# Performance work log

Measured on AMD Instinct MI355X. Metric: run time of the kernel, lower is better.

Reference implementation:

```python
import jax, jax.numpy as jnp
import numpy as np

B, T, D = 2, 2048, 2048
NH, NKV, HD = 16, 4, 128
EPS = 1e-6
ROPE_THETA = 10000.0


def rms_norm(x, w):
    # per-head RMSNorm over the last (head_dim) axis
    var = jnp.mean(jnp.square(x), axis=-1, keepdims=True)
    return x * jax.lax.rsqrt(var + EPS) * w


def rope_sin_cos(seq_len, dim, dtype):
    inv_freq = 1.0 / (ROPE_THETA ** (jnp.arange(0, dim, 2, dtype=jnp.float32) / dim))
    t = jnp.arange(seq_len, dtype=jnp.float32)
    ang = jnp.outer(t, inv_freq)                      # [T, HD/2]
    ang = jnp.concatenate([ang, ang], axis=-1)         # [T, HD]
    return jnp.sin(ang).astype(dtype), jnp.cos(ang).astype(dtype)


def rotate_half(x):
    x1, x2 = jnp.split(x, 2, axis=-1)
    return jnp.concatenate([-x2, x1], axis=-1)


def apply_rope(x, sin, cos):
    # x: [B, T, H, HD]; sin/cos: [T, HD]
    s = sin[None, :, None, :]
    c = cos[None, :, None, :]
    return x * c + rotate_half(x) * s


def setup_inputs() -> dict:
    key = jax.random.key(0)
    ks = jax.random.split(key, 5)
    scale = 1.0 / np.sqrt(D)
    return {
        "x": jax.random.normal(ks[0], (B, T, D), jnp.float32),
        "wq": jax.random.normal(ks[1], (D, D), jnp.float32) * scale,
        "wk": jax.random.normal(ks[2], (NKV * HD, D), jnp.float32) * scale,
        "wv": jax.random.normal(ks[3], (NKV * HD, D), jnp.float32) * scale,
        "wo": jax.random.normal(ks[4], (D, D), jnp.float32) * scale,
        "q_norm_w": jnp.ones((HD,), jnp.float32),
        "k_norm_w": jnp.ones((HD,), jnp.float32),
    }


def reference(x, wq, wk, wv, wo, q_norm_w, k_norm_w):
    b, t, _ = x.shape
    q = (x @ wq.T).reshape(b, t, NH, HD)    # [B,T,NH,HD]
    k = (x @ wk.T).reshape(b, t, NKV, HD)   # [B,T,NKV,HD]
    v = (x @ wv.T).reshape(b, t, NKV, HD)

    # per-head QK RMS norm
    q = rms_norm(q, q_norm_w)
    k = rms_norm(k, k_norm_w)

    # RoPE
    sin, cos = rope_sin_cos(t, HD, x.dtype)
    q = apply_rope(q, sin, cos)
    k = apply_rope(k, sin, cos)

    # GQA: expand kv heads to match query heads
    rep = NH // NKV
    k = jnp.repeat(k, rep, axis=2)          # [B,T,NH,HD]
    v = jnp.repeat(v, rep, axis=2)

    # causal SDPA
    scale = 1.0 / np.sqrt(HD)
    scores = jnp.einsum('bqhd,bkhd->bhqk', q, k) * scale
    causal = jnp.tril(jnp.ones((t, t), bool))
    scores = jnp.where(causal[None, None], scores, jnp.finfo(scores.dtype).min)
    probs = jax.nn.softmax(scores, axis=-1)
    att = jnp.einsum('bhqk,bkhd->bqhd', probs, v).reshape(b, t, NH * HD)
    return att @ wo.T
```

## Files before the change

### kernel.cpp

```cpp
#include <hip/hip_runtime.h>
#include <hip/hip_bf16.h>

#define B_ 2
#define T_ 2048
#define D_ 2048
#define NH_ 16
#define NKV_ 4
#define HD_ 128

using bf16 = __bf16;
using bf16x8 = __attribute__((ext_vector_type(8))) __bf16;
using bf16x4 = __attribute__((ext_vector_type(4))) __bf16;
using f32x4 = __attribute__((ext_vector_type(4))) float;

__device__ __forceinline__ void gld_lds16(bf16* lds, const bf16* g) {
  __builtin_amdgcn_global_load_lds(
      (const __attribute__((address_space(1))) void*)g,
      (__attribute__((address_space(3))) void*)lds, 16, 0, 0);
}

__global__ __launch_bounds__(256) void cvt_all(const float* __restrict__ x,
                                               const float* __restrict__ wq,
                                               const float* __restrict__ wk,
                                               const float* __restrict__ wv,
                                               const float* __restrict__ wo,
                                               bf16* __restrict__ xb,
                                               bf16* __restrict__ wqkvb,
                                               bf16* __restrict__ wob) {
  const int bid = blockIdx.x;
  const float* src;
  bf16* dst;
  int base;
  if (bid < 8192)       { src = x;  dst = xb;              base = bid; }
  else if (bid < 12288) { src = wq; dst = wqkvb;           base = bid - 8192; }
  else if (bid < 13312) { src = wk; dst = wqkvb + 4194304; base = bid - 12288; }
  else if (bid < 14336) { src = wv; dst = wqkvb + 5242880; base = bid - 13312; }
  else                  { src = wo; dst = wob;             base = bid - 14336; }
  const int i = base * 256 + threadIdx.x;
  float4 v = ((const float4*)src)[i];
  bf16x4 o;
  o[0] = (bf16)v.x; o[1] = (bf16)v.y; o[2] = (bf16)v.z; o[3] = (bf16)v.w;
  ((bf16x4*)dst)[i] = o;
}

template<typename OutT>
__global__ __launch_bounds__(256) void gemm_bt(const bf16* __restrict__ A,
                                               const bf16* __restrict__ Bt,
                                               OutT* __restrict__ C,
                                               int M, int N, int K) {
  __shared__ bf16 As[3][128 * 32];
  __shared__ bf16 Bs[3][128 * 32];
  const int tid = threadIdx.x;
  const int wid = tid >> 6;
  const int lane = tid & 63;
  const int g = lane >> 4, r = lane & 15;
  const int wm = wid >> 1, wn = wid & 1;
  const int gx = gridDim.x;
  const int nwg = gx * gridDim.y;
  const int flat = blockIdx.y * gx + blockIdx.x;
  const int swz = (flat & 7) * (nwg >> 3) + (flat >> 3);
  const long bm = (long)(swz / gx) * 128, bn = (long)(swz % gx) * 128;
  f32x4 acc[4][4] = {};
  const int NT = K >> 5;

  auto stage = [&](int buf, int k0) {
    for (int c = 0; c < 2; ++c) {
      int ch = wid * 2 + c;
      int row = ch * 16 + (lane >> 2);
      int col = (lane & 3) * 8;
      gld_lds16(&As[buf][ch * 512], A + (bm + row) * K + k0 + col);
      gld_lds16(&Bs[buf][ch * 512], Bt + (bn + row) * K + k0 + col);
    }
  };

  stage(0, 0);
  stage(1, 32);
  for (int t = 0; t < NT; ++t) {
    if (t + 1 < NT)
      asm volatile("s_waitcnt vmcnt(4)" ::: "memory");
    else
      asm volatile("s_waitcnt vmcnt(0)" ::: "memory");
    __builtin_amdgcn_s_barrier();
    if (t + 2 < NT) stage((t + 2) % 3, (t + 2) * 32);
    const bf16* as = As[t % 3];
    const bf16* bs = Bs[t % 3];
    bf16x8 af[4], bfr[4];
    for (int m = 0; m < 4; ++m)
      af[m] = *(const bf16x8*)(as + (wm * 64 + m * 16 + r) * 32 + g * 8);
    for (int n = 0; n < 4; ++n)
      bfr[n] = *(const bf16x8*)(bs + (wn * 64 + n * 16 + r) * 32 + g * 8);
    for (int m = 0; m < 4; ++m)
      for (int n = 0; n < 4; ++n)
        acc[m][n] = __builtin_amdgcn_mfma_f32_16x16x32_bf16(af[m], bfr[n], acc[m][n], 0, 0, 0);
  }

  for (int m = 0; m < 4; ++m)
    for (int n = 0; n < 4; ++n)
      for (int e = 0; e < 4; ++e) {
        long row = bm + wm * 64 + m * 16 + g * 4 + e;
        long col = bn + wn * 64 + n * 16 + r;
        C[row * N + col] = (OutT)acc[m][n][e];
      }
}

template<int IS_K>
__global__ __launch_bounds__(256) void norm_rope(const bf16* __restrict__ qkv,
                                                 const float* __restrict__ w,
                                                 bf16* __restrict__ out) {
  const int lane = threadIdx.x & 63;
  const int rloc = threadIdx.x >> 6;
  const int NHH = IS_K ? NKV_ : NH_;
  const int COFF = IS_K ? 2048 : 0;
  const long rid = (long)blockIdx.x * 4 + rloc;
  const int h = (int)(rid % NHH);
  const long bt = rid / NHH;
  const int t = (int)(bt % T_);
  const bf16* src = qkv + bt * 3072 + COFF + h * HD_;
  float v0 = (float)src[lane];
  float v1 = (float)src[lane + 64];
  float ss = v0 * v0 + v1 * v1;
  for (int o = 1; o < 64; o <<= 1) ss += __shfl_xor(ss, o, 64);
  float inv = rsqrtf(ss * (1.f / HD_) + 1e-6f);
  float n0 = v0 * inv * w[lane];
  float n1 = v1 * inv * w[lane + 64];
  float ang = (float)t * exp2f((float)lane * (-13.287712379549449f / 64.f));
  float sv, cv;
  __sincosf(ang, &sv, &cv);
  float o0 = n0 * cv - n1 * sv;
  float o1 = n1 * cv + n0 * sv;
  bf16* dst;
  if (IS_K) {
    long b = bt / T_;
    dst = out + ((b * NKV_ + h) * (long)T_ + t) * HD_;
  } else {
    dst = out + (bt * NH_ + h) * HD_;
  }
  dst[lane] = (bf16)o0;
  dst[lane + 64] = (bf16)o1;
}

__global__ __launch_bounds__(256) void vpack(const bf16* __restrict__ qkv,
                                             bf16* __restrict__ Vt) {
  __shared__ float tile[64][65];
  const int tt = blockIdx.x;
  const int dd = blockIdx.y & 1;
  const int bkv = blockIdx.y >> 1;
  const long b = bkv >> 2;
  const int kv = bkv & 3;
  const int t0 = tt * 64, d0 = dd * 64;
  for (int i = 0; i < 2; ++i) {
    int row = i * 32 + (threadIdx.x >> 3);
    int c8 = (threadIdx.x & 7) * 8;
    bf16x8 v = *(const bf16x8*)&qkv[(b * T_ + t0 + row) * 3072 + 2560 + kv * HD_ + d0 + c8];
    for (int j = 0; j < 8; ++j) tile[row][c8 + j] = (float)v[j];
  }
  __syncthreads();
  for (int i = 0; i < 2; ++i) {
    int drow = i * 32 + (threadIdx.x >> 3);
    int tc8 = (threadIdx.x & 7) * 8;
    bf16x8 o;
    for (int j = 0; j < 8; ++j) o[j] = (bf16)tile[tc8 + j][drow];
    *(bf16x8*)&Vt[((b * NKV_ + kv) * (long)HD_ + d0 + drow) * T_ + t0 + tc8] = o;
  }
}

__global__ __launch_bounds__(512) void flash_attn(const bf16* __restrict__ Q,
                                                  const bf16* __restrict__ K,
                                                  const bf16* __restrict__ V,
                                                  bf16* __restrict__ O) {
  __shared__ bf16 Ks[2][64 * 128];
  __shared__ bf16 Vs[2][128 * 64];
  __shared__ bf16 Ps[8][16 * 64];
  const int h = blockIdx.y, b = blockIdx.z;
  const int qt = b ? blockIdx.x : (gridDim.x - 1) - blockIdx.x;
  const int kv = h >> 2;
  const int tid = threadIdx.x, wid = tid >> 6, lane = tid & 63;
  const int g = lane >> 4, r = lane & 15;
  const int q0 = qt * 128;
  const int qbase = q0 + wid * 16;
  const int q = qbase + r;

  bf16x8 aq[4];
  const bf16* qp = Q + ((long)(b * T_ + q)) * (NH_ * HD_) + h * HD_;
  for (int kk = 0; kk < 4; ++kk) aq[kk] = *(const bf16x8*)(qp + kk * 32 + g * 8);

  f32x4 oacc[8] = {};
  float m_run = -1e30f, l_run = 0.f;

  const bf16* Kbase = K + ((long)(b * NKV_ + kv)) * T_ * HD_;
  const bf16* Vbase = V + ((long)(b * NKV_ + kv)) * (long)HD_ * T_;
  const int nkt = 2 * qt + 2;

  auto stageKV = [&](int buf, int k0) {
    for (int c = 0; c < 2; ++c) {
      int ch = wid * 2 + c;
      {
        int row = ch * 4 + (lane >> 4);
        int srccol = ((lane & 15) ^ (row & 7)) * 8;
        gld_lds16(&Ks[buf][ch * 512], Kbase + (long)(k0 + row) * HD_ + srccol);
      }
      {
        int row = ch * 8 + (lane >> 3);
        int srccol = ((lane & 7) ^ (row & 7)) * 8;
        gld_lds16(&Vs[buf][ch * 512], Vbase + (long)row * T_ + k0 + srccol);
      }
    }
  };

  stageKV(0, 0);
  for (int kt = 0; kt < nkt; ++kt) {
    const int k0 = kt * 64;
    const int cur = kt & 1;
    if (kt + 1 < nkt) {
      stageKV(cur ^ 1, k0 + 64);
      asm volatile("s_waitcnt vmcnt(4)" ::: "memory");
    } else {
      asm volatile("s_waitcnt vmcnt(0)" ::: "memory");
    }
    __builtin_amdgcn_s_barrier();

    f32x4 s[4] = {};
    __builtin_amdgcn_s_setprio(1);
    for (int n = 0; n < 4; ++n)
      for (int kk = 0; kk < 4; ++kk) {
        int row = n * 16 + r;
        bf16x8 bk = *(const bf16x8*)(&Ks[cur][row * 128 + (((kk * 4 + g) ^ (row & 7)) * 8)]);
        s[n] = __builtin_amdgcn_mfma_f32_16x16x32_bf16(bk, aq[kk], s[n], 0, 0, 0);
      }
    __builtin_amdgcn_s_setprio(0);

    const float scale = 0.088388347648318447f;
    const bool domask = (k0 + 63 > qbase);
    float mx = -1e30f;
    if (domask) {
      for (int n = 0; n < 4; ++n) {
        const int km = k0 + n * 16 + g * 4;
        for (int e = 0; e < 4; ++e) {
          float v = s[n][e] * scale;
          if (km + e > q) v = -1e30f;
          s[n][e] = v;
          mx = fmaxf(mx, v);
        }
      }
    } else {
      for (int n = 0; n < 4; ++n)
        for (int e = 0; e < 4; ++e) {
          float v = s[n][e] * scale;
          s[n][e] = v;
          mx = fmaxf(mx, v);
        }
    }
    mx = fmaxf(mx, __shfl_xor(mx, 16, 64));
    mx = fmaxf(mx, __shfl_xor(mx, 32, 64));
    float mnew = fmaxf(m_run, mx);
    float alpha = __expf(m_run - mnew);
    float ls = 0.f;
    for (int n = 0; n < 4; ++n) {
      bf16x4 pb;
      for (int e = 0; e < 4; ++e) {
        float p = __expf(s[n][e] - mnew);
        ls += p;
        pb[e] = (bf16)p;
      }
      int c = n * 2 + (g >> 1);
      *(bf16x4*)(&Ps[wid][r * 64 + ((c ^ (r & 7)) * 8) + (g & 1) * 4]) = pb;
    }
    ls += __shfl_xor(ls, 16, 64);
    ls += __shfl_xor(ls, 32, 64);
    m_run = mnew;
    l_run = l_run * alpha + ls;

    float al[4];
    for (int e = 0; e < 4; ++e)
      al[e] = __shfl(alpha, (lane & 48) | (g * 4 + e), 64);
    for (int dt = 0; dt < 8; ++dt)
      for (int e = 0; e < 4; ++e) oacc[dt][e] *= al[e];

    asm volatile("s_waitcnt lgkmcnt(0)" ::: "memory");

    __builtin_amdgcn_s_setprio(1);
    for (int kk = 0; kk < 2; ++kk) {
      bf16x8 ap = *(const bf16x8*)(&Ps[wid][r * 64 + (((kk * 4 + g) ^ (r & 7)) * 8)]);
      for (int dt = 0; dt < 8; ++dt) {
        int row = dt * 16 + r;
        bf16x8 bv = *(const bf16x8*)(&Vs[cur][row * 64 + (((kk * 4 + g) ^ (row & 7)) * 8)]);
        oacc[dt] = __builtin_amdgcn_mfma_f32_16x16x32_bf16(ap, bv, oacc[dt], 0, 0, 0);
      }
    }
    __builtin_amdgcn_s_setprio(0);
    __builtin_amdgcn_s_barrier();
  }

  float li[4];
  for (int e = 0; e < 4; ++e) {
    float lv = __shfl(l_run, (lane & 48) | (g * 4 + e), 64);
    li[e] = 1.f / lv;
  }
  for (int e = 0; e < 4; ++e) {
    const int grow = q0 + wid * 16 + g * 4 + e;
    bf16* dst = O + ((long)(b * T_ + grow)) * (NH_ * HD_) + h * HD_;
    for (int dt = 0; dt < 8; ++dt)
      dst[dt * 16 + r] = (bf16)(oacc[dt][e] * li[e]);
  }
}

extern "C" void kernel_launch(void* const* d_in, const int* in_sizes, int n_in,
                              void* d_out, int out_size, void* d_ws, size_t ws_size,
                              hipStream_t stream) {
  const float* x  = (const float*)d_in[0];
  const float* wq = (const float*)d_in[1];
  const float* wk = (const float*)d_in[2];
  const float* wv = (const float*)d_in[3];
  const float* wo = (const float*)d_in[4];
  const float* qw = (const float*)d_in[5];
  const float* kw = (const float*)d_in[6];
  float* out = (float*)d_out;

  char* p = (char*)d_ws;
  bf16* xb    = (bf16*)(p);
  bf16* wqkvb = (bf16*)(p + 16777216);
  bf16* wob   = (bf16*)(p + 29360128);
  bf16* QKVr  = (bf16*)(p + 37748736);
  bf16* Qb    = (bf16*)(p + 62914560);
  bf16* Kb    = (bf16*)(p + 79691776);
  bf16* Vt    = (bf16*)(p + 83886080);
  bf16* attb  = (bf16*)(p + 88080384);

  cvt_all<<<18432, 256, 0, stream>>>(x, wq, wk, wv, wo, xb, wqkvb, wob);

  gemm_bt<bf16><<<dim3(24, 32), 256, 0, stream>>>(xb, wqkvb, QKVr, 4096, 3072, 2048);

  norm_rope<0><<<16384, 256, 0, stream>>>(QKVr, qw, Qb);
  norm_rope<1><<<4096, 256, 0, stream>>>(QKVr, kw, Kb);
  vpack<<<dim3(32, 16), 256, 0, stream>>>(QKVr, Vt);

  flash_attn<<<dim3(16, 16, 2), 512, 0, stream>>>(Qb, Kb, Vt, attb);

  gemm_bt<float><<<dim3(16, 32), 256, 0, stream>>>(attb, wob, out, 4096, 2048, 2048);
}
```

Before: 218.0 us.

## Split flash-attn softmax into two half-tile passes and merge Q/K norm-rope launches

Result: slower. 224.9 us (+3.2%).

```diff
diff --git a/kernel.cpp b/kernel.cpp
--- a/kernel.cpp
+++ b/kernel.cpp
@@ -103,15 +103,19 @@
       }
 }
 
-template<int IS_K>
-__global__ __launch_bounds__(256) void norm_rope(const bf16* __restrict__ qkv,
-                                                 const float* __restrict__ w,
-                                                 bf16* __restrict__ out) {
+__global__ __launch_bounds__(256) void norm_rope_qk(const bf16* __restrict__ qkv,
+                                                    const float* __restrict__ qw,
+                                                    const float* __restrict__ kw,
+                                                    bf16* __restrict__ Qb,
+                                                    bf16* __restrict__ Kb) {
   const int lane = threadIdx.x & 63;
   const int rloc = threadIdx.x >> 6;
+  const int bid = blockIdx.x;
+  const int IS_K = bid >= 16384;
   const int NHH = IS_K ? NKV_ : NH_;
   const int COFF = IS_K ? 2048 : 0;
-  const long rid = (long)blockIdx.x * 4 + rloc;
+  const float* w = IS_K ? kw : qw;
+  const long rid = (long)(IS_K ? bid - 16384 : bid) * 4 + rloc;
   const int h = (int)(rid % NHH);
   const long bt = rid / NHH;
   const int t = (int)(bt % T_);
@@ -131,9 +135,9 @@
   bf16* dst;
   if (IS_K) {
     long b = bt / T_;
-    dst = out + ((b * NKV_ + h) * (long)T_ + t) * HD_;
+    dst = Kb + ((b * NKV_ + h) * (long)T_ + t) * HD_;
   } else {
-    dst = out + (bt * NH_ + h) * HD_;
+    dst = Qb + (bt * NH_ + h) * HD_;
   }
   dst[lane] = (bf16)o0;
   dst[lane + 64] = (bf16)o1;
@@ -231,63 +235,64 @@
 
     const float scale = 0.088388347648318447f;
     const bool domask = (k0 + 63 > qbase);
-    float mx = -1e30f;
-    if (domask) {
-      for (int n = 0; n < 4; ++n) {
-        const int km = k0 + n * 16 + g * 4;
+
+    for (int hh = 0; hh < 2; ++hh) {
+      float mx = -1e30f;
+      if (domask) {
+        for (int n = 2 * hh; n < 2 * hh + 2; ++n) {
+          const int km = k0 + n * 16 + g * 4;
+          for (int e = 0; e < 4; ++e) {
+            float v = s[n][e] * scale;
+            if (km + e > q) v = -1e30f;
+            s[n][e] = v;
+            mx = fmaxf(mx, v);
+          }
+        }
+      } else {
+        for (int n = 2 * hh; n < 2 * hh + 2; ++n)
+          for (int e = 0; e < 4; ++e) {
+            float v = s[n][e] * scale;
+            s[n][e] = v;
+            mx = fmaxf(mx, v);
+          }
+      }
+      mx = fmaxf(mx, __shfl_xor(mx, 16, 64));
+      mx = fmaxf(mx, __shfl_xor(mx, 32, 64));
+      float mnew = fmaxf(m_run, mx);
+      float alpha = __expf(m_run - mnew);
+      float ls = 0.f;
+      for (int n = 2 * hh; n < 2 * hh + 2; ++n) {
+        bf16x4 pb;
         for (int e = 0; e < 4; ++e) {
-          float v = s[n][e] * scale;
-          if (km + e > q) v = -1e30f;
-          s[n][e] = v;
-          mx = fmaxf(mx, v);
+          float p = __expf(s[n][e] - mnew);
+          ls += p;
+          pb[e] = (bf16)p;
         }
-      }
-    } else {
-      for (int n = 0; n < 4; ++n)
-        for (int e = 0; e < 4; ++e) {
-          float v = s[n][e] * scale;
-          s[n][e] = v;
-          mx = fmaxf(mx, v);
-        }
-    }
-    mx = fmaxf(mx, __shfl_xor(mx, 16, 64));
-    mx = fmaxf(mx, __shfl_xor(mx, 32, 64));
-    float mnew = fmaxf(m_run, mx);
-    float alpha = __expf(m_run - mnew);
-    float ls = 0.f;
-    for (int n = 0; n < 4; ++n) {
-      bf16x4 pb;
-      for (int e = 0; e < 4; ++e) {
-        float p = __expf(s[n][e] - mnew);
-        ls += p;
-        pb[e] = (bf16)p;
-      }
-      int c = n * 2 + (g >> 1);
-      *(bf16x4*)(&Ps[wid][r * 64 + ((c ^ (r & 7)) * 8) + (g & 1) * 4]) = pb;
-    }
-    ls += __shfl_xor(ls, 16, 64);
-    ls += __shfl_xor(ls, 32, 64);
-    m_run = mnew;
-    l_run = l_run * alpha + ls;
-
-    float al[4];
-    for (int e = 0; e < 4; ++e)
-      al[e] = __shfl(alpha, (lane & 48) | (g * 4 + e), 64);
-    for (int dt = 0; dt < 8; ++dt)
-      for (int e = 0; e < 4; ++e) oacc[dt][e] *= al[e];
-
-    asm volatile("s_waitcnt lgkmcnt(0)" ::: "memory");
-
-    __builtin_amdgcn_s_setprio(1);
-    for (int kk = 0; kk < 2; ++kk) {
-      bf16x8 ap = *(const bf16x8*)(&Ps[wid][r * 64 + (((kk * 4 + g) ^ (r & 7)) * 8)]);
+        int c = n * 2 + (g >> 1);
+        *(bf16x4*)(&Ps[wid][r * 64 + ((c ^ (r & 7)) * 8) + (g & 1) * 4]) = pb;
+      }
+      ls += __shfl_xor(ls, 16, 64);
+      ls += __shfl_xor(ls, 32, 64);
+      m_run = mnew;
+      l_run = l_run * alpha + ls;
+
+      float al[4];
+      for (int e = 0; e < 4; ++e)
+        al[e] = __shfl(alpha, (lane & 48) | (g * 4 + e), 64);
+      for (int dt = 0; dt < 8; ++dt)
+        for (int e = 0; e < 4; ++e) oacc[dt][e] *= al[e];
+
+      asm volatile("s_waitcnt lgkmcnt(0)" ::: "memory");
+
+      __builtin_amdgcn_s_setprio(1);
+      bf16x8 ap = *(const bf16x8*)(&Ps[wid][r * 64 + (((hh * 4 + g) ^ (r & 7)) * 8)]);
       for (int dt = 0; dt < 8; ++dt) {
         int row = dt * 16 + r;
-        bf16x8 bv = *(const bf16x8*)(&Vs[cur][row * 64 + (((kk * 4 + g) ^ (row & 7)) * 8)]);
+        bf16x8 bv = *(const bf16x8*)(&Vs[cur][row * 64 + (((hh * 4 + g) ^ (row & 7)) * 8)]);
         oacc[dt] = __builtin_amdgcn_mfma_f32_16x16x32_bf16(ap, bv, oacc[dt], 0, 0, 0);
       }
+      __builtin_amdgcn_s_setprio(0);
     }
-    __builtin_amdgcn_s_setprio(0);
     __builtin_amdgcn_s_barrier();
   }
 
@@ -330,8 +335,7 @@
 
   gemm_bt<bf16><<<dim3(24, 32), 256, 0, stream>>>(xb, wqkvb, QKVr, 4096, 3072, 2048);
 
-  norm_rope<0><<<16384, 256, 0, stream>>>(QKVr, qw, Qb);
-  norm_rope<1><<<4096, 256, 0, stream>>>(QKVr, kw, Kb);
+  norm_rope_qk<<<20480, 256, 0, stream>>>(QKVr, qw, kw, Qb, Kb);
   vpack<<<dim3(32, 16), 256, 0, stream>>>(QKVr, Vt);
 
   flash_attn<<<dim3(16, 16, 2), 512, 0, stream>>>(Qb, Kb, Vt, attb);
```

## Fuse Q norm+RoPE into flash attention and merge K-prep with V transpose

Applied to the files above, without the earlier changes.

New measurement: 207.2 us (median of 4 runs). 5.0% less time.

```diff
diff --git a/kernel.cpp b/kernel.cpp
--- a/kernel.cpp
+++ b/kernel.cpp
@@ -103,68 +103,62 @@
       }
 }
 
-template<int IS_K>
-__global__ __launch_bounds__(256) void norm_rope(const bf16* __restrict__ qkv,
-                                                 const float* __restrict__ w,
-                                                 bf16* __restrict__ out) {
-  const int lane = threadIdx.x & 63;
-  const int rloc = threadIdx.x >> 6;
-  const int NHH = IS_K ? NKV_ : NH_;
-  const int COFF = IS_K ? 2048 : 0;
-  const long rid = (long)blockIdx.x * 4 + rloc;
-  const int h = (int)(rid % NHH);
-  const long bt = rid / NHH;
-  const int t = (int)(bt % T_);
-  const bf16* src = qkv + bt * 3072 + COFF + h * HD_;
-  float v0 = (float)src[lane];
-  float v1 = (float)src[lane + 64];
-  float ss = v0 * v0 + v1 * v1;
-  for (int o = 1; o < 64; o <<= 1) ss += __shfl_xor(ss, o, 64);
-  float inv = rsqrtf(ss * (1.f / HD_) + 1e-6f);
-  float n0 = v0 * inv * w[lane];
-  float n1 = v1 * inv * w[lane + 64];
-  float ang = (float)t * exp2f((float)lane * (-13.287712379549449f / 64.f));
-  float sv, cv;
-  __sincosf(ang, &sv, &cv);
-  float o0 = n0 * cv - n1 * sv;
-  float o1 = n1 * cv + n0 * sv;
-  bf16* dst;
-  if (IS_K) {
+__global__ __launch_bounds__(256) void prep_kv(const bf16* __restrict__ qkv,
+                                               const float* __restrict__ kw,
+                                               bf16* __restrict__ Kb,
+                                               bf16* __restrict__ Vt) {
+  __shared__ float tile[64][65];
+  const int bid = blockIdx.x;
+  if (bid < 4096) {
+    const int lane = threadIdx.x & 63;
+    const int rloc = threadIdx.x >> 6;
+    const long rid = (long)bid * 4 + rloc;
+    const int h = (int)(rid % NKV_);
+    const long bt = rid / NKV_;
+    const int t = (int)(bt % T_);
+    const bf16* src = qkv + bt * 3072 + 2048 + h * HD_;
+    float v0 = (float)src[lane];
+    float v1 = (float)src[lane + 64];
+    float ss = v0 * v0 + v1 * v1;
+    for (int o = 1; o < 64; o <<= 1) ss += __shfl_xor(ss, o, 64);
+    float inv = rsqrtf(ss * (1.f / HD_) + 1e-6f);
+    float n0 = v0 * inv * kw[lane];
+    float n1 = v1 * inv * kw[lane + 64];
+    float ang = (float)t * exp2f((float)lane * (-13.287712379549449f / 64.f));
+    float sv, cv;
+    __sincosf(ang, &sv, &cv);
     long b = bt / T_;
-    dst = out + ((b * NKV_ + h) * (long)T_ + t) * HD_;
+    bf16* dst = Kb + ((b * NKV_ + h) * (long)T_ + t) * HD_;
+    dst[lane] = (bf16)(n0 * cv - n1 * sv);
+    dst[lane + 64] = (bf16)(n1 * cv + n0 * sv);
   } else {
-    dst = out + (bt * NH_ + h) * HD_;
-  }
-  dst[lane] = (bf16)o0;
-  dst[lane + 64] = (bf16)o1;
-}
-
-__global__ __launch_bounds__(256) void vpack(const bf16* __restrict__ qkv,
-                                             bf16* __restrict__ Vt) {
-  __shared__ float tile[64][65];
-  const int tt = blockIdx.x;
-  const int dd = blockIdx.y & 1;
-  const int bkv = blockIdx.y >> 1;
-  const long b = bkv >> 2;
-  const int kv = bkv & 3;
-  const int t0 = tt * 64, d0 = dd * 64;
-  for (int i = 0; i < 2; ++i) {
-    int row = i * 32 + (threadIdx.x >> 3);
-    int c8 = (threadIdx.x & 7) * 8;
-    bf16x8 v = *(const bf16x8*)&qkv[(b * T_ + t0 + row) * 3072 + 2560 + kv * HD_ + d0 + c8];
-    for (int j = 0; j < 8; ++j) tile[row][c8 + j] = (float)v[j];
-  }
-  __syncthreads();
-  for (int i = 0; i < 2; ++i) {
-    int drow = i * 32 + (threadIdx.x >> 3);
-    int tc8 = (threadIdx.x & 7) * 8;
-    bf16x8 o;
-    for (int j = 0; j < 8; ++j) o[j] = (bf16)tile[tc8 + j][drow];
-    *(bf16x8*)&Vt[((b * NKV_ + kv) * (long)HD_ + d0 + drow) * T_ + t0 + tc8] = o;
-  }
-}
-
-__global__ __launch_bounds__(512) void flash_attn(const bf16* __restrict__ Q,
+    const int bid2 = bid - 4096;
+    const int tt = bid2 & 31;
+    const int by = bid2 >> 5;
+    const int dd = by & 1;
+    const int bkv = by >> 1;
+    const long b = bkv >> 2;
+    const int kv = bkv & 3;
+    const int t0 = tt * 64, d0 = dd * 64;
+    for (int i = 0; i < 2; ++i) {
+      int row = i * 32 + (threadIdx.x >> 3);
+      int c8 = (threadIdx.x & 7) * 8;
+      bf16x8 v = *(const bf16x8*)&qkv[(b * T_ + t0 + row) * 3072 + 2560 + kv * HD_ + d0 + c8];
+      for (int j = 0; j < 8; ++j) tile[row][c8 + j] = (float)v[j];
+    }
+    __syncthreads();
+    for (int i = 0; i < 2; ++i) {
+      int drow = i * 32 + (threadIdx.x >> 3);
+      int tc8 = (threadIdx.x & 7) * 8;
+      bf16x8 o;
+      for (int j = 0; j < 8; ++j) o[j] = (bf16)tile[tc8 + j][drow];
+      *(bf16x8*)&Vt[((b * NKV_ + kv) * (long)HD_ + d0 + drow) * T_ + t0 + tc8] = o;
+    }
+  }
+}
+
+__global__ __launch_bounds__(512) void flash_attn(const bf16* __restrict__ QKV,
+                                                  const float* __restrict__ qw,
                                                   const bf16* __restrict__ K,
                                                   const bf16* __restrict__ V,
                                                   bf16* __restrict__ O) {
@@ -180,9 +174,33 @@
   const int qbase = q0 + wid * 16;
   const int q = qbase + r;
 
+  const bf16* qsrc = QKV + ((long)(b * T_ + q)) * 3072 + h * HD_;
+  float ss = 0.f;
+  for (int kk = 0; kk < 4; ++kk) {
+    bf16x8 tq = *(const bf16x8*)(qsrc + kk * 32 + g * 8);
+    for (int j = 0; j < 8; ++j) { float f = (float)tq[j]; ss += f * f; }
+  }
+  ss += __shfl_xor(ss, 16, 64);
+  ss += __shfl_xor(ss, 32, 64);
+  const float inv = rsqrtf(ss * (1.f / HD_) + 1e-6f);
   bf16x8 aq[4];
-  const bf16* qp = Q + ((long)(b * T_ + q)) * (NH_ * HD_) + h * HD_;
-  for (int kk = 0; kk < 4; ++kk) aq[kk] = *(const bf16x8*)(qp + kk * 32 + g * 8);
+  for (int kk = 0; kk < 2; ++kk) {
+    bf16x8 tlo = *(const bf16x8*)(qsrc + kk * 32 + g * 8);
+    bf16x8 thi = *(const bf16x8*)(qsrc + kk * 32 + 64 + g * 8);
+    bf16x8 alo, ahi;
+    for (int j = 0; j < 8; ++j) {
+      const int d = kk * 32 + g * 8 + j;
+      float n0 = (float)tlo[j] * inv * qw[d];
+      float n1 = (float)thi[j] * inv * qw[d + 64];
+      float ang = (float)q * exp2f((float)d * (-13.287712379549449f / 64.f));
+      float sv, cv;
+      __sincosf(ang, &sv, &cv);
+      alo[j] = (bf16)(n0 * cv - n1 * sv);
+      ahi[j] = (bf16)(n1 * cv + n0 * sv);
+    }
+    aq[kk] = alo;
+    aq[kk + 2] = ahi;
+  }
 
   f32x4 oacc[8] = {};
   float m_run = -1e30f, l_run = 0.f;
@@ -321,7 +339,6 @@
   bf16* wqkvb = (bf16*)(p + 16777216);
   bf16* wob   = (bf16*)(p + 29360128);
   bf16* QKVr  = (bf16*)(p + 37748736);
-  bf16* Qb    = (bf16*)(p + 62914560);
   bf16* Kb    = (bf16*)(p + 79691776);
   bf16* Vt    = (bf16*)(p + 83886080);
   bf16* attb  = (bf16*)(p + 88080384);
@@ -330,11 +347,9 @@
 
   gemm_bt<bf16><<<dim3(24, 32), 256, 0, stream>>>(xb, wqkvb, QKVr, 4096, 3072, 2048);
 
-  norm_rope<0><<<16384, 256, 0, stream>>>(QKVr, qw, Qb);
-  norm_rope<1><<<4096, 256, 0, stream>>>(QKVr, kw, Kb);
-  vpack<<<dim3(32, 16), 256, 0, stream>>>(QKVr, Vt);
-
-  flash_attn<<<dim3(16, 16, 2), 512, 0, stream>>>(Qb, Kb, Vt, attb);
+  prep_kv<<<4608, 256, 0, stream>>>(QKVr, kw, Kb, Vt);
+
+  flash_attn<<<dim3(16, 16, 2), 512, 0, stream>>>(QKVr, qw, Kb, Vt, attb);
 
   gemm_bt<float><<<dim3(16, 32), 256, 0, stream>>>(attb, wob, out, 4096, 2048, 2048);
 }
```
